# Optimization experiments

Hardware: AMD Instinct MI355X
Metric: run time of the kernel (lower is better)

The kernel has to match this reference:

```python
import jax, jax.numpy as jnp
import numpy as np

EPS = 1e-9
N, E = 100000, 1000000
IN_F, OUT_F, HEADS = 128, 64, 2


def normalize_points(x):
    # UHG projective normalize: unit-norm spatial part, keep last (homogeneous) coord
    n = jnp.linalg.norm(x[..., :-1], axis=-1, keepdims=True)
    return jnp.concatenate([x[..., :-1] / jnp.maximum(n, EPS), x[..., -1:]], axis=-1)


def uhg_inner(a, b):
    # hyperbolic inner product: spatial dot minus time-time product
    return jnp.sum(a[..., :-1] * b[..., :-1], axis=-1) - a[..., -1] * b[..., -1]


def compute_cross_ratio(p1, p2, p3, p4):
    num = uhg_inner(p1, p3) * uhg_inner(p2, p4)
    den = uhg_inner(p1, p4) * uhg_inner(p2, p3)
    return num / jnp.where(jnp.abs(den) < EPS, EPS, den)


def restore_cross_ratio(x, cr_target):
    cr_cur = compute_cross_ratio(x[0], x[1], x[2], x[3])
    scale = jnp.abs(cr_target / jnp.where(jnp.abs(cr_cur) < EPS, EPS, cr_cur)) ** 0.25
    return x * scale


def setup_inputs() -> dict:
    key = jax.random.key(0)
    ks = jax.random.split(key, 10)
    s_in = 1.0 / np.sqrt(IN_F)
    s_hid = 1.0 / np.sqrt(OUT_F * HEADS)
    H = OUT_F * HEADS
    return {
        "x": jax.random.normal(ks[0], (N, IN_F), dtype=jnp.float32),
        "edge_index": jax.random.randint(ks[1], (2, E), 0, N, dtype=jnp.int64),
        "Wq": jax.random.uniform(ks[2], (H, IN_F), jnp.float32, -s_in, s_in),
        "bq": jnp.zeros((H,), jnp.float32),
        "Wk": jax.random.uniform(ks[3], (H, IN_F), jnp.float32, -s_in, s_in),
        "bk": jnp.zeros((H,), jnp.float32),
        "Wv": jax.random.uniform(ks[4], (H, IN_F), jnp.float32, -s_in, s_in),
        "bv": jnp.zeros((H,), jnp.float32),
        "Wo": jax.random.uniform(ks[5], (OUT_F, H), jnp.float32, -s_hid, s_hid),
        "bo": jnp.zeros((OUT_F,), jnp.float32),
    }


def reference(x, edge_index, Wq, bq, Wk, bk, Wv, bv, Wo, bo):
    n = x.shape[0]
    cr_initial = compute_cross_ratio(x[0], x[1], x[2], x[3])
    x_proj = normalize_points(x)
    q = (x_proj @ Wq.T + bq).reshape(n, HEADS, OUT_F)
    k = (x_proj @ Wk.T + bk).reshape(n, HEADS, OUT_F)
    v = (x_proj @ Wv.T + bv).reshape(n, HEADS, OUT_F)
    row, col = edge_index[0], edge_index[1]
    qe = normalize_points(q[row])  # [E, H, D]
    ke = normalize_points(k[col])
    scores = uhg_inner(qe, ke) / np.sqrt(IN_F)  # [E, H]
    alpha = jax.nn.softmax(scores, axis=0)  # global softmax over edges (as in source)
    msgs = v[col] * alpha[..., None]  # [E, H, D]
    out = jax.ops.segment_sum(msgs, row, num_segments=n)  # [N, H, D]
    out = out.reshape(n, HEADS * OUT_F)
    out = out @ Wo.T + bo
    out = restore_cross_ratio(out, cr_initial)
    return out
```

## Files before the change

### kernel.cpp

```cpp
#include <hip/hip_runtime.h>
#include <math.h>

#define EPSF 1e-9f
#define INV_SQRT128 0.08838834764831845f

typedef _Float16 half8 __attribute__((ext_vector_type(8)));
typedef float f32x4 __attribute__((ext_vector_type(4)));

__device__ __forceinline__ void gl_lds16(const void* g, void* l) {
    __builtin_amdgcn_global_load_lds((const __attribute__((address_space(1))) void*)g,
                                     (__attribute__((address_space(3))) void*)l, 16, 0, 0);
}

__global__ void k_wpack(const float* __restrict__ Wq, const float* __restrict__ Wk,
                        const float* __restrict__ Wv, half8* __restrict__ whi,
                        half8* __restrict__ wlo, float* __restrict__ w127) {
    int t = blockIdx.x * 256 + threadIdx.x;
    if (t >= 6144) return;
    int col = t & 127, g = (t >> 7) & 3, ks = (t >> 9) & 3, kind = t >> 11;
    const float* W = (kind == 0) ? Wq : (kind == 1) ? Wk : Wv;
    const float4* W4 = (const float4*)W;
    float4 a = W4[col * 32 + ks * 8 + g * 2];
    float4 b = W4[col * 32 + ks * 8 + g * 2 + 1];
    float xv[8] = {a.x, a.y, a.z, a.w, b.x, b.y, b.z, b.w};
    half8 h, lo;
#pragma unroll
    for (int j = 0; j < 8; j++) {
        _Float16 hh = (_Float16)xv[j];
        h[j] = hh;
        lo[j] = (_Float16)((xv[j] - (float)hh) * 4096.0f);
    }
    whi[t] = h;
    wlo[t] = lo;
    if (ks == 3 && g == 3) w127[kind * 128 + col] = xv[7];
}

__global__ void k_wpack2(const float* __restrict__ Wo, half8* __restrict__ wohi,
                         half8* __restrict__ wolo) {
    int t = blockIdx.x * 256 + threadIdx.x;
    if (t >= 1024) return;
    int col = t & 63, g = (t >> 6) & 3, ks = t >> 8;
    const float4* W4 = (const float4*)Wo;
    float4 a = W4[col * 32 + ks * 8 + g * 2];
    float4 b = W4[col * 32 + ks * 8 + g * 2 + 1];
    float xv[8] = {a.x, a.y, a.z, a.w, b.x, b.y, b.z, b.w};
    half8 h, lo;
#pragma unroll
    for (int j = 0; j < 8; j++) {
        _Float16 hh = (_Float16)xv[j];
        h[j] = hh;
        lo[j] = (_Float16)((xv[j] - (float)hh) * 4096.0f);
    }
    wohi[t] = h;
    wolo[t] = lo;
}

__global__ void __launch_bounds__(256, 2)
k_qkvm(const float* __restrict__ x,
       const half8* __restrict__ whi, const half8* __restrict__ wlo,
       const float* __restrict__ w127,
       const float* __restrict__ bq, const float* __restrict__ bk,
       const float* __restrict__ bv,
       float* __restrict__ qn, float* __restrict__ kvout, int N) {
    __shared__ half8 bsh[4096];

    int tid = threadIdx.x;
    int wv = tid >> 6;
    int l = tid & 63;
    int r = l & 15;
    int g = l >> 4;
    int rowbase = blockIdx.x * 128 + wv * 32;
    const float4* x4 = (const float4*)x;

    {
        const half8* sH = whi + wv * 512;
        const half8* sL = wlo + wv * 512;
#pragma unroll
        for (int i = 0; i < 8; i++) {
            gl_lds16(sH + i * 64 + l, bsh + wv * 512 + i * 64);
            gl_lds16(sL + i * 64 + l, bsh + 2048 + wv * 512 + i * 64);
        }
    }

    half8 hiA[2][4], loA[2][4];
    float rnj[2][4], tcj[2][4];
#pragma unroll
    for (int t = 0; t < 2; t++) {
        int row = min(rowbase + t * 16 + r, N - 1);
        float ssum = 0.f, tl = 0.f;
#pragma unroll
        for (int ks = 0; ks < 4; ks++) {
            float4 a = x4[(size_t)row * 32 + ks * 8 + g * 2];
            float4 bb = x4[(size_t)row * 32 + ks * 8 + g * 2 + 1];
            float xv[8] = {a.x, a.y, a.z, a.w, bb.x, bb.y, bb.z, bb.w};
#pragma unroll
            for (int j = 0; j < 8; j++) {
                _Float16 hh = (_Float16)xv[j];
                hiA[t][ks][j] = hh;
                loA[t][ks][j] = (_Float16)((xv[j] - (float)hh) * 4096.0f);
                ssum += xv[j] * xv[j];
            }
            if (ks == 3 && g == 3) { tl = xv[7]; ssum -= xv[7] * xv[7]; }
        }
        ssum += __shfl_xor(ssum, 16);
        ssum += __shfl_xor(ssum, 32);
        float rn = 1.f / fmaxf(sqrtf(ssum), EPSF);
        float tla = __shfl(tl, 48 + r);
        float tc = tla * (1.f - rn);
#pragma unroll
        for (int j = 0; j < 4; j++) {
            rnj[t][j] = __shfl(rn, g * 4 + j);
            tcj[t][j] = __shfl(tc, g * 4 + j);
        }
    }

    asm volatile("s_waitcnt vmcnt(0)" ::: "memory");
    __syncthreads();

    const float* const bks[3] = {bq, bk, bv};
    bool lane15 = (r == 15);
    const f32x4 zz = {0.f, 0.f, 0.f, 0.f};
    int dsbase = g * 128 + r;

    for (int kind = 0; kind < 3; kind++) {
        float wcA[2][4], bbA[2][4];
#pragma unroll
        for (int h = 0; h < 2; h++)
#pragma unroll
            for (int ct = 0; ct < 4; ct++) {
                int col = (h * 4 + ct) * 16 + r;
                wcA[h][ct] = w127[kind * 128 + col];
                bbA[h][ct] = bks[kind][col];
            }

#pragma unroll
        for (int h = 0; h < 2; h++) {
            f32x4 aM[2][4], aX[2][4];
#pragma unroll
            for (int t = 0; t < 2; t++)
#pragma unroll
                for (int ct = 0; ct < 4; ct++) { aM[t][ct] = zz; aX[t][ct] = zz; }

#pragma unroll
            for (int ks = 0; ks < 4; ks++) {
                half8 hB[4], lB[4];
#pragma unroll
                for (int ct = 0; ct < 4; ct++) {
                    int bi = dsbase + ks * 512 + (h * 4 + ct) * 16;
                    hB[ct] = bsh[bi];
                    lB[ct] = bsh[2048 + bi];
                }
#pragma unroll
                for (int ct = 0; ct < 4; ct++) {
                    aM[0][ct] = __builtin_amdgcn_mfma_f32_16x16x32_f16(hiA[0][ks], hB[ct], aM[0][ct], 0, 0, 0);
                    aM[1][ct] = __builtin_amdgcn_mfma_f32_16x16x32_f16(hiA[1][ks], hB[ct], aM[1][ct], 0, 0, 0);
                    aX[0][ct] = __builtin_amdgcn_mfma_f32_16x16x32_f16(hiA[0][ks], lB[ct], aX[0][ct], 0, 0, 0);
                    aX[0][ct] = __builtin_amdgcn_mfma_f32_16x16x32_f16(loA[0][ks], hB[ct], aX[0][ct], 0, 0, 0);
                    aX[1][ct] = __builtin_amdgcn_mfma_f32_16x16x32_f16(hiA[1][ks], lB[ct], aX[1][ct], 0, 0, 0);
                    aX[1][ct] = __builtin_amdgcn_mfma_f32_16x16x32_f16(loA[1][ks], hB[ct], aX[1][ct], 0, 0, 0);
                }
            }

#pragma unroll
            for (int t = 0; t < 2; t++) {
                float cv[4][4];
#pragma unroll
                for (int ct = 0; ct < 4; ct++)
#pragma unroll
                    for (int j = 0; j < 4; j++) {
                        float acc = aM[t][ct][j] + aX[t][ct][j] * (1.0f / 4096.0f);
                        cv[ct][j] = fmaf(rnj[t][j], acc, fmaf(tcj[t][j], wcA[h][ct], bbA[h][ct]));
                    }
                if (kind < 2) {
#pragma unroll
                    for (int j = 0; j < 4; j++) {
                        float ss = 0.f;
#pragma unroll
                        for (int ct = 0; ct < 4; ct++) {
                            float c = cv[ct][j];
                            ss += (ct == 3 && lane15) ? 0.f : c * c;
                        }
                        ss += __shfl_xor(ss, 1);
                        ss += __shfl_xor(ss, 2);
                        ss += __shfl_xor(ss, 4);
                        ss += __shfl_xor(ss, 8);
                        float rh = 1.f / fmaxf(sqrtf(ss), EPSF);
#pragma unroll
                        for (int ct = 0; ct < 4; ct++) {
                            bool ist = (ct == 3) && lane15;
                            if (!ist) cv[ct][j] *= rh;
                            if (kind == 0) {
                                if (ist) cv[ct][j] = -cv[ct][j];
                                cv[ct][j] *= INV_SQRT128;
                            }
                        }
                    }
                }
#pragma unroll
                for (int j = 0; j < 4; j++) {
                    int row = rowbase + t * 16 + g * 4 + j;
                    if (row < N) {
                        float* dst = (kind == 0)
                            ? (qn + (size_t)row * 128)
                            : (kvout + (size_t)row * 256 + (kind == 2 ? 128 : 0));
#pragma unroll
                        for (int ct = 0; ct < 4; ct++)
                            dst[(h * 4 + ct) * 16 + r] = cv[ct][j];
                    }
                }
            }
        }

        if (kind < 2) {
            __syncthreads();
            const half8* sH = whi + (kind + 1) * 2048 + wv * 512;
            const half8* sL = wlo + (kind + 1) * 2048 + wv * 512;
#pragma unroll
            for (int i = 0; i < 8; i++) {
                gl_lds16(sH + i * 64 + l, bsh + wv * 512 + i * 64);
                gl_lds16(sL + i * 64 + l, bsh + 2048 + wv * 512 + i * 64);
            }
            asm volatile("s_waitcnt vmcnt(0)" ::: "memory");
            __syncthreads();
        }
    }
}

__global__ void k_bin1(const int* __restrict__ ei, int* __restrict__ bcnt,
                       int E, int chunk) {
    __shared__ int h[256];
    int t = threadIdx.x, b = blockIdx.x;
    h[t] = 0;
    __syncthreads();
    int s = b * chunk, e1 = min(s + chunk, E);
    for (int e = s + t; e < e1; e += 256) atomicAdd(&h[ei[e] >> 9], 1);
    __syncthreads();
    bcnt[b * 256 + t] = h[t];
}

__global__ void k_bin2(int* __restrict__ bcnt, int* __restrict__ bintot) {
    __shared__ int sd[256];
    int b = blockIdx.x, t = threadIdx.x;
    int v = bcnt[t * 256 + b];
    sd[t] = v;
    __syncthreads();
    for (int off = 1; off < 256; off <<= 1) {
        int val = sd[t];
        int add = (t >= off) ? sd[t - off] : 0;
        __syncthreads();
        sd[t] = val + add;
        __syncthreads();
    }
    bcnt[t * 256 + b] = sd[t] - v;
    if (t == 255) bintot[b] = sd[255];
}

__global__ void k_bin3(const int* __restrict__ bintot, int* __restrict__ binoff,
                       int* __restrict__ offs, int N, int E) {
    __shared__ int sd[256];
    int t = threadIdx.x;
    int v = bintot[t];
    sd[t] = v;
    __syncthreads();
    for (int off = 1; off < 256; off <<= 1) {
        int val = sd[t];
        int add = (t >= off) ? sd[t - off] : 0;
        __syncthreads();
        sd[t] = val + add;
        __syncthreads();
    }
    binoff[t] = sd[t] - v;
    if (t == 255) {
        binoff[256] = sd[255];
        offs[N] = E;
    }
}

__global__ void k_scat1(const int* __restrict__ ei, const int* __restrict__ bcnt,
                        const int* __restrict__ binoff, int* __restrict__ packed,
                        int E, int chunk) {
    __shared__ int cur[256];
    int t = threadIdx.x, b = blockIdx.x;
    cur[t] = binoff[t] + bcnt[b * 256 + t];
    __syncthreads();
    int s = b * chunk, e1 = min(s + chunk, E);
    for (int e = s + t; e < e1; e += 256) {
        int r = ei[e];
        int c = ei[E + e];
        int p = atomicAdd(&cur[r >> 9], 1);
        packed[p] = ((r & 511) << 17) | c;
    }
}

__global__ void __launch_bounds__(256)
k_sortf(const int* __restrict__ packed, const int* __restrict__ binoff,
        int* __restrict__ ccol, int* __restrict__ offs, int N) {
    __shared__ int seg[6656];
    __shared__ int h[512];
    __shared__ int sc[256];
    int b = blockIdx.x, t = threadIdx.x;
    int s = binoff[b], e1 = binoff[b + 1];
    int cnt = min(e1 - s, 6656);
    for (int i = t; i < cnt; i += 256) seg[i] = packed[s + i];
    h[t] = 0;
    h[t + 256] = 0;
    __syncthreads();
    for (int i = t; i < cnt; i += 256) atomicAdd(&h[seg[i] >> 17], 1);
    __syncthreads();
    int v0 = h[2 * t], v1 = h[2 * t + 1];
    int pair = v0 + v1;
    sc[t] = pair;
    __syncthreads();
    for (int off = 1; off < 256; off <<= 1) {
        int val = sc[t];
        int add = (t >= off) ? sc[t - off] : 0;
        __syncthreads();
        sc[t] = val + add;
        __syncthreads();
    }
    int pexcl = sc[t] - pair;
    __syncthreads();
    h[2 * t] = pexcl;
    h[2 * t + 1] = pexcl + v0;
    int rowbase = b << 9;
    if (rowbase + 2 * t < N) offs[rowbase + 2 * t] = s + h[2 * t];
    if (rowbase + 2 * t + 1 < N) offs[rowbase + 2 * t + 1] = s + h[2 * t + 1];
    __syncthreads();
    for (int i = t; i < cnt; i += 256) {
        int pk = seg[i];
        int p = atomicAdd(&h[pk >> 17], 1);
        ccol[s + p] = pk & 0x1FFFF;
    }
}

__global__ void k_edge(const float* __restrict__ qn, const float* __restrict__ kv,
                       const int* __restrict__ offs, const int* __restrict__ ccol,
                       float* __restrict__ U, double* __restrict__ psum, int N) {
    int g = threadIdx.x >> 5;
    int l = threadIdx.x & 31;
    int head = l >> 4;
    int n = blockIdx.x * 8 + g;
    double esum = 0.0;
    if (n < N) {
        float4 q4 = ((const float4*)qn)[(size_t)n * 32 + l];
        int s0 = offs[n], s1 = offs[n + 1];
        float4 acc = {0.f, 0.f, 0.f, 0.f};
        const float4* kv4 = (const float4*)kv;
        int i = s0;
        for (; i + 4 <= s1; i += 4) {
            int c0 = ccol[i];
            int c1 = ccol[i + 1];
            int c2 = ccol[i + 2];
            int c3 = ccol[i + 3];
            float4 ka = kv4[(size_t)c0 * 64 + l];
            float4 va = kv4[(size_t)c0 * 64 + 32 + l];
            float4 kb = kv4[(size_t)c1 * 64 + l];
            float4 vb = kv4[(size_t)c1 * 64 + 32 + l];
            float4 kc = kv4[(size_t)c2 * 64 + l];
            float4 vc = kv4[(size_t)c2 * 64 + 32 + l];
            float4 kd = kv4[(size_t)c3 * 64 + l];
            float4 vd = kv4[(size_t)c3 * 64 + 32 + l];
            float p0 = q4.x * ka.x;
            p0 = fmaf(q4.y, ka.y, p0); p0 = fmaf(q4.z, ka.z, p0); p0 = fmaf(q4.w, ka.w, p0);
            float p1 = q4.x * kb.x;
            p1 = fmaf(q4.y, kb.y, p1); p1 = fmaf(q4.z, kb.z, p1); p1 = fmaf(q4.w, kb.w, p1);
            float p2 = q4.x * kc.x;
            p2 = fmaf(q4.y, kc.y, p2); p2 = fmaf(q4.z, kc.z, p2); p2 = fmaf(q4.w, kc.w, p2);
            float p3 = q4.x * kd.x;
            p3 = fmaf(q4.y, kd.y, p3); p3 = fmaf(q4.z, kd.z, p3); p3 = fmaf(q4.w, kd.w, p3);
            p0 += __shfl_xor(p0, 1); p1 += __shfl_xor(p1, 1);
            p2 += __shfl_xor(p2, 1); p3 += __shfl_xor(p3, 1);
            p0 += __shfl_xor(p0, 2); p1 += __shfl_xor(p1, 2);
            p2 += __shfl_xor(p2, 2); p3 += __shfl_xor(p3, 2);
            p0 += __shfl_xor(p0, 4); p1 += __shfl_xor(p1, 4);
            p2 += __shfl_xor(p2, 4); p3 += __shfl_xor(p3, 4);
            p0 += __shfl_xor(p0, 8); p1 += __shfl_xor(p1, 8);
            p2 += __shfl_xor(p2, 8); p3 += __shfl_xor(p3, 8);
            float e0 = expf(p0);
            float e1 = expf(p1);
            float e2 = expf(p2);
            float e3 = expf(p3);
            acc.x = fmaf(va.x, e0, acc.x); acc.y = fmaf(va.y, e0, acc.y);
            acc.z = fmaf(va.z, e0, acc.z); acc.w = fmaf(va.w, e0, acc.w);
            acc.x = fmaf(vb.x, e1, acc.x); acc.y = fmaf(vb.y, e1, acc.y);
            acc.z = fmaf(vb.z, e1, acc.z); acc.w = fmaf(vb.w, e1, acc.w);
            acc.x = fmaf(vc.x, e2, acc.x); acc.y = fmaf(vc.y, e2, acc.y);
            acc.z = fmaf(vc.z, e2, acc.z); acc.w = fmaf(vc.w, e2, acc.w);
            acc.x = fmaf(vd.x, e3, acc.x); acc.y = fmaf(vd.y, e3, acc.y);
            acc.z = fmaf(vd.z, e3, acc.z); acc.w = fmaf(vd.w, e3, acc.w);
            esum += (double)((e0 + e1) + (e2 + e3));
        }
        for (; i < s1; i++) {
            int c = ccol[i];
            float4 k4 = kv4[(size_t)c * 64 + l];
            float4 v4 = kv4[(size_t)c * 64 + 32 + l];
            float p = q4.x * k4.x;
            p = fmaf(q4.y, k4.y, p); p = fmaf(q4.z, k4.z, p); p = fmaf(q4.w, k4.w, p);
            p += __shfl_xor(p, 1);
            p += __shfl_xor(p, 2);
            p += __shfl_xor(p, 4);
            p += __shfl_xor(p, 8);
            float e = expf(p);
            acc.x = fmaf(v4.x, e, acc.x); acc.y = fmaf(v4.y, e, acc.y);
            acc.z = fmaf(v4.z, e, acc.z); acc.w = fmaf(v4.w, e, acc.w);
            esum += (double)e;
        }
        ((float4*)U)[(size_t)n * 32 + l] = acc;
    }
    __shared__ double sd[2][8];
    if ((l & 15) == 0) sd[head][g] = esum;
    __syncthreads();
    if (threadIdx.x < 2) {
        double s = 0.0;
        for (int i2 = 0; i2 < 8; i2++) s += sd[threadIdx.x][i2];
        psum[(size_t)blockIdx.x * 2 + threadIdx.x] = s;
    }
}

__global__ void k_sum2(const double* __restrict__ psum, double* __restrict__ sumf, int P) {
    double s0 = 0.0, s1 = 0.0;
    for (int i = threadIdx.x; i < P; i += blockDim.x) {
        s0 += psum[2 * i];
        s1 += psum[2 * i + 1];
    }
    for (int off = 32; off; off >>= 1) {
        s0 += __shfl_xor(s0, off);
        s1 += __shfl_xor(s1, off);
    }
    __shared__ double sd[2][4];
    int w = threadIdx.x >> 6;
    if ((threadIdx.x & 63) == 0) { sd[0][w] = s0; sd[1][w] = s1; }
    __syncthreads();
    if (threadIdx.x == 0) {
        for (int i = 1; i < 4; i++) { s0 += sd[0][i]; s1 += sd[1][i]; }
        sumf[0] = s0;
        sumf[1] = s1;
    }
}

__global__ void k_crout4(const float* __restrict__ x, const float* __restrict__ U,
                         const float* __restrict__ Wo, const float* __restrict__ bo,
                         const double* __restrict__ sumf, float* __restrict__ scalef) {
    __shared__ float xs[4 * 128];
    __shared__ float o4[4 * 64];
    __shared__ double crin_sh;
    int tid = threadIdx.x;
    xs[tid] = U[tid];
    xs[tid + 256] = U[tid + 256];
    if (tid < 64) {
        int l = tid;
        const int pa[4] = {0, 1, 0, 1};
        const int pb[4] = {2, 3, 3, 2};
        double inner[4];
        for (int p = 0; p < 4; p++) {
            const float* a = x + pa[p] * 128;
            const float* b = x + pb[p] * 128;
            double s = (double)a[l] * (double)b[l];
            double t = (double)a[l + 64] * (double)b[l + 64];
            s += (l == 63) ? -t : t;
            for (int off = 32; off; off >>= 1) s += __shfl_xor(s, off);
            inner[p] = s;
        }
        if (l == 0) {
            double num = inner[0] * inner[1];
            double den = inner[2] * inner[3];
            if (fabs(den) < 1e-9) den = 1e-9;
            crin_sh = num / den;
        }
    }
    __syncthreads();
    int w = tid >> 6, o = tid & 63;
    float si0 = (float)(1.0 / sumf[0]);
    float si1 = (float)(1.0 / sumf[1]);
    const float* xr = xs + w * 128;
    const float* wr = Wo + (size_t)o * 128;
    float d0 = 0.f, d1 = 0.f;
    for (int j = 0; j < 64; j++) d0 = fmaf(xr[j], wr[j], d0);
    for (int j = 64; j < 128; j++) d1 = fmaf(xr[j], wr[j], d1);
    o4[w * 64 + o] = d0 * si0 + d1 * si1 + bo[o];
    __syncthreads();
    if (tid < 64) {
        int l = tid;
        const int pa[4] = {0, 1, 0, 1};
        const int pb[4] = {2, 3, 3, 2};
        double inner[4];
        for (int p = 0; p < 4; p++) {
            double t = (double)o4[pa[p] * 64 + l] * (double)o4[pb[p] * 64 + l];
            if (l == 63) t = -t;
            for (int off = 32; off; off >>= 1) t += __shfl_xor(t, off);
            inner[p] = t;
        }
        if (l == 0) {
            double num = inner[0] * inner[1];
            double den = inner[2] * inner[3];
            if (fabs(den) < 1e-9) den = 1e-9;
            double crc = num / den;
            if (fabs(crc) < 1e-9) crc = 1e-9;
            double ratio = crin_sh / crc;
            scalef[0] = (float)pow(fabs(ratio), 0.25);
        }
    }
}

__global__ void __launch_bounds__(256, 2)
k_outm(const float* __restrict__ U, const half8* __restrict__ wohi,
       const half8* __restrict__ wolo, const float* __restrict__ bo,
       const double* __restrict__ sumf, const float* __restrict__ scalef,
       float* __restrict__ out, int N) {
    __shared__ half8 bsh[2048];
    int tid = threadIdx.x;
    int wv = tid >> 6;
    int l = tid & 63;
    int r = l & 15;
    int g = l >> 4;
    int rowbase = blockIdx.x * 128 + wv * 32;

    {
        const half8* sH = wohi + wv * 256;
        const half8* sL = wolo + wv * 256;
#pragma unroll
        for (int i = 0; i < 4; i++) {
            gl_lds16(sH + i * 64 + l, bsh + wv * 256 + i * 64);
            gl_lds16(sL + i * 64 + l, bsh + 1024 + wv * 256 + i * 64);
        }
    }

    float si0 = (float)(1.0 / sumf[0]);
    float si1 = (float)(1.0 / sumf[1]);
    const float4* U4 = (const float4*)U;
    half8 hiA[2][4], loA[2][4];
#pragma unroll
    for (int t = 0; t < 2; t++) {
        int row = min(rowbase + t * 16 + r, N - 1);
#pragma unroll
        for (int ks = 0; ks < 4; ks++) {
            float si = (ks < 2) ? si0 : si1;
            float4 a = U4[(size_t)row * 32 + ks * 8 + g * 2];
            float4 b = U4[(size_t)row * 32 + ks * 8 + g * 2 + 1];
            float xv[8] = {a.x, a.y, a.z, a.w, b.x, b.y, b.z, b.w};
#pragma unroll
            for (int j = 0; j < 8; j++) {
                float v = xv[j] * si;
                _Float16 hh = (_Float16)v;
                hiA[t][ks][j] = hh;
                loA[t][ks][j] = (_Float16)((v - (float)hh) * 4096.0f);
            }
        }
    }

    asm volatile("s_waitcnt vmcnt(0)" ::: "memory");
    __syncthreads();

    const f32x4 zz = {0.f, 0.f, 0.f, 0.f};
    f32x4 aM[2][4], aX[2][4];
#pragma unroll
    for (int t = 0; t < 2; t++)
#pragma unroll
        for (int ct = 0; ct < 4; ct++) { aM[t][ct] = zz; aX[t][ct] = zz; }

#pragma unroll
    for (int ks = 0; ks < 4; ks++) {
        half8 hB[4], lB[4];
#pragma unroll
        for (int ct = 0; ct < 4; ct++) {
            int bi = ks * 256 + g * 64 + ct * 16 + r;
            hB[ct] = bsh[bi];
            lB[ct] = bsh[1024 + bi];
        }
#pragma unroll
        for (int ct = 0; ct < 4; ct++) {
            aM[0][ct] = __builtin_amdgcn_mfma_f32_16x16x32_f16(hiA[0][ks], hB[ct], aM[0][ct], 0, 0, 0);
            aM[1][ct] = __builtin_amdgcn_mfma_f32_16x16x32_f16(hiA[1][ks], hB[ct], aM[1][ct], 0, 0, 0);
            aX[0][ct] = __builtin_amdgcn_mfma_f32_16x16x32_f16(hiA[0][ks], lB[ct], aX[0][ct], 0, 0, 0);
            aX[0][ct] = __builtin_amdgcn_mfma_f32_16x16x32_f16(loA[0][ks], hB[ct], aX[0][ct], 0, 0, 0);
            aX[1][ct] = __builtin_amdgcn_mfma_f32_16x16x32_f16(hiA[1][ks], lB[ct], aX[1][ct], 0, 0, 0);
            aX[1][ct] = __builtin_amdgcn_mfma_f32_16x16x32_f16(loA[1][ks], hB[ct], aX[1][ct], 0, 0, 0);
        }
    }

    float sf = scalef[0];
#pragma unroll
    for (int t = 0; t < 2; t++)
#pragma unroll
        for (int ct = 0; ct < 4; ct++) {
            float bb = bo[ct * 16 + r];
#pragma unroll
            for (int j = 0; j < 4; j++) {
                int row = rowbase + t * 16 + g * 4 + j;
                if (row < N) {
                    float c = (aM[t][ct][j] + aX[t][ct][j] * (1.0f / 4096.0f) + bb) * sf;
                    out[(size_t)row * 64 + ct * 16 + r] = c;
                }
            }
        }
}

extern "C" void kernel_launch(void* const* d_in, const int* in_sizes, int n_in,
                              void* d_out, int out_size, void* d_ws, size_t ws_size,
                              hipStream_t stream) {
    const float* x  = (const float*)d_in[0];
    const int*   ei = (const int*)d_in[1];
    const float* Wq = (const float*)d_in[2];
    const float* bq = (const float*)d_in[3];
    const float* Wk = (const float*)d_in[4];
    const float* bk = (const float*)d_in[5];
    const float* Wv = (const float*)d_in[6];
    const float* bv = (const float*)d_in[7];
    const float* Wo = (const float*)d_in[8];
    const float* bo = (const float*)d_in[9];
    float* out = (float*)d_out;

    const int N = in_sizes[0] / 128;
    const int E = in_sizes[1] / 2;
    const size_t NR = (size_t)N * 128;
    const int NGB = (N + 127) / 128;
    const int GB = (N + 7) / 8;
    const int NBK1 = 256;
    const int chunk = (E + NBK1 - 1) / NBK1;
    const int NBINS = (N + 511) >> 9;

    float* qn = (float*)d_ws;
    float* kv = qn + NR;
    int* offs = (int*)(kv + NR * 2);
    int* ccol = offs + N + 2;
    int* bcnt = ccol + E;
    int* bintot = bcnt + 256 * 256;
    int* binoff = bintot + 256;
    uintptr_t pd = ((uintptr_t)(binoff + 257 + 1) + 7) & ~(uintptr_t)7;
    double* psum = (double*)pd;
    double* sumf = psum + (size_t)GB * 2;
    float* scalef = (float*)(sumf + 2);

    uintptr_t pw = ((uintptr_t)ccol + 15) & ~(uintptr_t)15;
    half8* whi = (half8*)pw;
    half8* wlo = whi + 6144;
    float* w127 = (float*)(wlo + 6144);

    uintptr_t pw2 = ((uintptr_t)bcnt + 15) & ~(uintptr_t)15;
    half8* wohi = (half8*)pw2;
    half8* wolo = wohi + 1024;

    float* U = qn;

    k_wpack<<<24, 256, 0, stream>>>(Wq, Wk, Wv, whi, wlo, w127);
    k_qkvm<<<NGB, 256, 0, stream>>>(x, whi, wlo, w127, bq, bk, bv, qn, kv, N);
    k_bin1<<<NBK1, 256, 0, stream>>>(ei, bcnt, E, chunk);
    k_bin2<<<256, 256, 0, stream>>>(bcnt, bintot);
    k_bin3<<<1, 256, 0, stream>>>(bintot, binoff, offs, N, E);
    k_scat1<<<NBK1, 256, 0, stream>>>(ei, bcnt, binoff, ccol, E, chunk);
    k_wpack2<<<4, 256, 0, stream>>>(Wo, wohi, wolo);
    k_sortf<<<NBINS, 256, 0, stream>>>(ccol, binoff, ccol, offs, N);
    k_edge<<<GB, 256, 0, stream>>>(qn, kv, offs, ccol, U, psum, N);
    k_sum2<<<1, 256, 0, stream>>>(psum, sumf, GB);
    k_crout4<<<1, 256, 0, stream>>>(x, U, Wo, bo, sumf, scalef);
    k_outm<<<NGB, 256, 0, stream>>>(U, wohi, wolo, bo, sumf, scalef, out, N);
}
```

Measured before the change: 413.3 us.

## Fuse edge histogram into QKV GEMM kernel and fold psum reduction into crout

The edge-bin histogram (k_bin1) now runs as interleaved odd blocks inside an enlarged 512-thread k_qkvm launch, so the memory-bound histogram overlaps with the GEMM blocks. The GEMM blocks now cover 256 rows each with 8 waves, and each wave stages half as much weight data into shared memory. Separately, the k_sum2 reduction is merged into k_crout4, removing one launch. The cost is a larger block with higher launch bounds, which puts register pressure on the GEMM path, and more complex block indexing.

```diff
diff --git a/kernel.cpp b/kernel.cpp
--- a/kernel.cpp
+++ b/kernel.cpp
@@ -55,30 +55,46 @@
     wolo[t] = lo;
 }
 
-__global__ void __launch_bounds__(256, 2)
+__global__ void __launch_bounds__(512, 4)
 k_qkvm(const float* __restrict__ x,
        const half8* __restrict__ whi, const half8* __restrict__ wlo,
        const float* __restrict__ w127,
        const float* __restrict__ bq, const float* __restrict__ bk,
        const float* __restrict__ bv,
-       float* __restrict__ qn, float* __restrict__ kvout, int N) {
+       float* __restrict__ qn, float* __restrict__ kvout,
+       const int* __restrict__ ei, int* __restrict__ bcnt,
+       int N, int E, int chunk) {
+    int b = (int)blockIdx.x;
     __shared__ half8 bsh[4096];
+    if (b < 512 && (b & 1)) {
+        __shared__ int h[256];
+        int t = threadIdx.x;
+        int hid = b >> 1;
+        if (t < 256) h[t] = 0;
+        __syncthreads();
+        int s = hid * chunk, e1 = min(s + chunk, E);
+        for (int e = s + t; e < e1; e += 512) atomicAdd(&h[ei[e] >> 9], 1);
+        __syncthreads();
+        if (t < 256) bcnt[hid * 256 + t] = h[t];
+        return;
+    }
+    int gb = (b < 512) ? (b >> 1) : (b - 256);
 
     int tid = threadIdx.x;
     int wv = tid >> 6;
     int l = tid & 63;
     int r = l & 15;
     int g = l >> 4;
-    int rowbase = blockIdx.x * 128 + wv * 32;
+    int rowbase = gb * 256 + wv * 32;
     const float4* x4 = (const float4*)x;
 
     {
-        const half8* sH = whi + wv * 512;
-        const half8* sL = wlo + wv * 512;
-#pragma unroll
-        for (int i = 0; i < 8; i++) {
-            gl_lds16(sH + i * 64 + l, bsh + wv * 512 + i * 64);
-            gl_lds16(sL + i * 64 + l, bsh + 2048 + wv * 512 + i * 64);
+        const half8* sH = whi + wv * 256;
+        const half8* sL = wlo + wv * 256;
+#pragma unroll
+        for (int i = 0; i < 4; i++) {
+            gl_lds16(sH + i * 64 + l, bsh + wv * 256 + i * 64);
+            gl_lds16(sL + i * 64 + l, bsh + 2048 + wv * 256 + i * 64);
         }
     }
 
@@ -213,29 +229,17 @@
 
         if (kind < 2) {
             __syncthreads();
-            const half8* sH = whi + (kind + 1) * 2048 + wv * 512;
-            const half8* sL = wlo + (kind + 1) * 2048 + wv * 512;
-#pragma unroll
-            for (int i = 0; i < 8; i++) {
-                gl_lds16(sH + i * 64 + l, bsh + wv * 512 + i * 64);
-                gl_lds16(sL + i * 64 + l, bsh + 2048 + wv * 512 + i * 64);
+            const half8* sH = whi + (kind + 1) * 2048 + wv * 256;
+            const half8* sL = wlo + (kind + 1) * 2048 + wv * 256;
+#pragma unroll
+            for (int i = 0; i < 4; i++) {
+                gl_lds16(sH + i * 64 + l, bsh + wv * 256 + i * 64);
+                gl_lds16(sL + i * 64 + l, bsh + 2048 + wv * 256 + i * 64);
             }
             asm volatile("s_waitcnt vmcnt(0)" ::: "memory");
             __syncthreads();
         }
     }
-}
-
-__global__ void k_bin1(const int* __restrict__ ei, int* __restrict__ bcnt,
-                       int E, int chunk) {
-    __shared__ int h[256];
-    int t = threadIdx.x, b = blockIdx.x;
-    h[t] = 0;
-    __syncthreads();
-    int s = b * chunk, e1 = min(s + chunk, E);
-    for (int e = s + t; e < e1; e += 256) atomicAdd(&h[ei[e] >> 9], 1);
-    __syncthreads();
-    bcnt[b * 256 + t] = h[t];
 }
 
 __global__ void k_bin2(int* __restrict__ bcnt, int* __restrict__ bintot) {
@@ -417,38 +421,39 @@
     }
 }
 
-__global__ void k_sum2(const double* __restrict__ psum, double* __restrict__ sumf, int P) {
-    double s0 = 0.0, s1 = 0.0;
-    for (int i = threadIdx.x; i < P; i += blockDim.x) {
-        s0 += psum[2 * i];
-        s1 += psum[2 * i + 1];
-    }
-    for (int off = 32; off; off >>= 1) {
-        s0 += __shfl_xor(s0, off);
-        s1 += __shfl_xor(s1, off);
-    }
-    __shared__ double sd[2][4];
-    int w = threadIdx.x >> 6;
-    if ((threadIdx.x & 63) == 0) { sd[0][w] = s0; sd[1][w] = s1; }
-    __syncthreads();
-    if (threadIdx.x == 0) {
-        for (int i = 1; i < 4; i++) { s0 += sd[0][i]; s1 += sd[1][i]; }
-        sumf[0] = s0;
-        sumf[1] = s1;
-    }
-}
-
 __global__ void k_crout4(const float* __restrict__ x, const float* __restrict__ U,
                          const float* __restrict__ Wo, const float* __restrict__ bo,
-                         const double* __restrict__ sumf, float* __restrict__ scalef) {
+                         const double* __restrict__ psum, int P,
+                         double* __restrict__ sumf, float* __restrict__ scalef) {
     __shared__ float xs[4 * 128];
     __shared__ float o4[4 * 64];
     __shared__ double crin_sh;
+    __shared__ double sdr[2][4];
     int tid = threadIdx.x;
+    {
+        double s0 = 0.0, s1 = 0.0;
+        for (int i = tid; i < P; i += 256) {
+            s0 += psum[2 * i];
+            s1 += psum[2 * i + 1];
+        }
+        for (int off = 32; off; off >>= 1) {
+            s0 += __shfl_xor(s0, off);
+            s1 += __shfl_xor(s1, off);
+        }
+        int w = tid >> 6;
+        if ((tid & 63) == 0) { sdr[0][w] = s0; sdr[1][w] = s1; }
+    }
     xs[tid] = U[tid];
     xs[tid + 256] = U[tid + 256];
-    if (tid < 64) {
-        int l = tid;
+    __syncthreads();
+    if (tid == 0) {
+        double s0 = sdr[0][0] + sdr[0][1] + sdr[0][2] + sdr[0][3];
+        double s1 = sdr[1][0] + sdr[1][1] + sdr[1][2] + sdr[1][3];
+        sumf[0] = s0;
+        sumf[1] = s1;
+    }
+    if (tid >= 64 && tid < 128) {
+        int l = tid - 64;
         const int pa[4] = {0, 1, 0, 1};
         const int pb[4] = {2, 3, 3, 2};
         double inner[4];
@@ -613,10 +618,10 @@
     const int N = in_sizes[0] / 128;
     const int E = in_sizes[1] / 2;
     const size_t NR = (size_t)N * 128;
+    const int NGB2 = (N + 255) / 256;
     const int NGB = (N + 127) / 128;
     const int GB = (N + 7) / 8;
-    const int NBK1 = 256;
-    const int chunk = (E + NBK1 - 1) / NBK1;
+    const int chunk = (E + 255) / 256;
     const int NBINS = (N + 511) >> 9;
 
     float* qn = (float*)d_ws;
@@ -643,15 +648,14 @@
     float* U = qn;
 
     k_wpack<<<24, 256, 0, stream>>>(Wq, Wk, Wv, whi, wlo, w127);
-    k_qkvm<<<NGB, 256, 0, stream>>>(x, whi, wlo, w127, bq, bk, bv, qn, kv, N);
-    k_bin1<<<NBK1, 256, 0, stream>>>(ei, bcnt, E, chunk);
+    k_qkvm<<<NGB2 + 256, 512, 0, stream>>>(x, whi, wlo, w127, bq, bk, bv,
+                                           qn, kv, ei, bcnt, N, E, chunk);
     k_bin2<<<256, 256, 0, stream>>>(bcnt, bintot);
     k_bin3<<<1, 256, 0, stream>>>(bintot, binoff, offs, N, E);
-    k_scat1<<<NBK1, 256, 0, stream>>>(ei, bcnt, binoff, ccol, E, chunk);
+    k_scat1<<<256, 256, 0, stream>>>(ei, bcnt, binoff, ccol, E, chunk);
     k_wpack2<<<4, 256, 0, stream>>>(Wo, wohi, wolo);
     k_sortf<<<NBINS, 256, 0, stream>>>(ccol, binoff, ccol, offs, N);
     k_edge<<<GB, 256, 0, stream>>>(qn, kv, offs, ccol, U, psum, N);
-    k_sum2<<<1, 256, 0, stream>>>(psum, sumf, GB);
-    k_crout4<<<1, 256, 0, stream>>>(x, U, Wo, bo, sumf, scalef);
+    k_crout4<<<1, 256, 0, stream>>>(x, U, Wo, bo, psum, GB, sumf, scalef);
     k_outm<<<NGB, 256, 0, stream>>>(U, wohi, wolo, bo, sumf, scalef, out, N);
 }
```

Result: slower. 547.5 us (+32.5%).
